# Optimization experiments

Measured on AMD Instinct MI355X. Metric: run time of the kernel, lower is better.

Reference implementation:

```python
import jax, jax.numpy as jnp
import numpy as np

SEQ, BATCH, IN, HID, OUT = 4096, 64, 64, 256, 1


def setup_inputs() -> dict:
    key = jax.random.key(0)
    ks = jax.random.split(key, 7)
    s = 1.0 / np.sqrt(HID)  # torch GRU/Linear init scale
    return {
        "x": jax.random.normal(ks[0], (SEQ, BATCH, IN), dtype=jnp.float32),
        "w_ih": jax.random.uniform(ks[1], (3 * HID, IN), jnp.float32, -s, s),
        "w_hh": jax.random.uniform(ks[2], (3 * HID, HID), jnp.float32, -s, s),
        "b_ih": jax.random.uniform(ks[3], (3 * HID,), jnp.float32, -s, s),
        "b_hh": jax.random.uniform(ks[4], (3 * HID,), jnp.float32, -s, s),
        "fc_w": jax.random.uniform(ks[5], (OUT, HID), jnp.float32, -s, s),
        "fc_b": jax.random.uniform(ks[6], (OUT,), jnp.float32, -s, s),
    }


def _gru(x, w_ih, w_hh, b_ih, b_hh):
    # x: [S, B, I]. Precompute input-side gate projections in one big GEMM.
    xg = jnp.einsum("sbi,gi->sbg", x, w_ih) + b_ih  # [S, B, 3H]
    H = w_hh.shape[1]
    h0 = jnp.zeros((x.shape[1], H), x.dtype)

    def step(h, xt):
        hg = h @ w_hh.T + b_hh  # [B, 3H]
        xr, xz, xn = jnp.split(xt, 3, axis=-1)
        hr, hz, hn = jnp.split(hg, 3, axis=-1)
        r = jax.nn.sigmoid(xr + hr)
        z = jax.nn.sigmoid(xz + hz)
        n = jnp.tanh(xn + r * hn)  # torch GRU: r gates the hidden-side n term
        h_new = (1.0 - z) * n + z * h
        return h_new, h_new

    _, hs = jax.lax.scan(step, h0, xg)  # hs: [S, B, H]
    return hs


def reference(x, w_ih, w_hh, b_ih, b_hh, fc_w, fc_b):
    hs = _gru(x, w_ih, w_hh, b_ih, b_hh)  # [S, B, H]
    out = hs @ fc_w.T + fc_b  # [S, B, OUT]
    # original does .squeeze(0): no-op since S != 1
    return out
```

## Files before the change

### kernel.cpp

```cpp
#include <hip/hip_runtime.h>

#define SEQ  4096
#define NB   64
#define NI   64
#define NH   256

typedef short  bf16x8 __attribute__((ext_vector_type(8)));
typedef short  bf16x4 __attribute__((ext_vector_type(4)));
typedef float  f32x4  __attribute__((ext_vector_type(4)));

__device__ __forceinline__ unsigned short f2bf(float f) {
    union { float f; unsigned u; } v; v.f = f;
    return (unsigned short)((v.u + 0x7fffu + ((v.u >> 16) & 1u)) >> 16);
}
__device__ __forceinline__ float bflo(int p) {
    union { int i; float f; } u; u.i = p << 16; return u.f;
}
__device__ __forceinline__ float bfhi(int p) {
    union { int i; float f; } u; u.i = p & 0xffff0000; return u.f;
}
__device__ __forceinline__ float fast_rcp(float x) { return __builtin_amdgcn_rcpf(x); }
__device__ __forceinline__ float sigm(float x) { return fast_rcp(1.f + __expf(-x)); }
__device__ __forceinline__ float tanh_(float x) {
    x = fminf(15.f, fmaxf(-15.f, x));
    float e = __expf(2.f * x);
    return (e - 1.f) * fast_rcp(e + 1.f);
}
__device__ __forceinline__ f32x4 mfma16(bf16x8 a, bf16x8 b, f32x4 c) {
    return __builtin_amdgcn_mfma_f32_16x16x32_bf16(a, b, c, 0, 0, 0);
}
__device__ __forceinline__ bf16x8 ldfrag(const float* p) {
    float4 a = *(const float4*)p;
    float4 b = *(const float4*)(p + 4);
    bf16x8 r;
    r[0] = (short)f2bf(a.x); r[1] = (short)f2bf(a.y);
    r[2] = (short)f2bf(a.z); r[3] = (short)f2bf(a.w);
    r[4] = (short)f2bf(b.x); r[5] = (short)f2bf(b.y);
    r[6] = (short)f2bf(b.z); r[7] = (short)f2bf(b.w);
    return r;
}

__global__ __launch_bounds__(1024) void xg_pre(
        const float* __restrict__ x, const float* __restrict__ w_ih,
        const float* __restrict__ b_ih, const float* __restrict__ b_hh,
        short* __restrict__ xg, size_t plane, int t0, int ns)
{
    const int tid = threadIdx.x, wv = tid >> 6, lane = tid & 63;
    const int nn = lane & 15, q = lane >> 4;
    const int jb = wv;

    bf16x8 w[3][2];
    float bias[3];
    #pragma unroll
    for (int g = 0; g < 3; ++g) {
        const int row = g * NH + jb * 16 + nn;
        w[g][0] = ldfrag(w_ih + row * NI + q * 8);
        w[g][1] = ldfrag(w_ih + row * NI + 32 + q * 8);
        bias[g] = b_ih[row] + (g < 2 ? b_hh[row] : 0.f);
    }

    const int NT = ns * 4;
    for (int rt = blockIdx.x; rt < NT; rt += gridDim.x) {
        const float* xr = x + ((size_t)t0 * NB + (size_t)rt * 16 + nn) * NI + q * 8;
        bf16x8 a0 = ldfrag(xr);
        bf16x8 a1 = ldfrag(xr + 32);
        #pragma unroll
        for (int g = 0; g < 3; ++g) {
            f32x4 acc = {0.f, 0.f, 0.f, 0.f};
            acc = mfma16(a0, w[g][0], acc);
            acc = mfma16(a1, w[g][1], acc);
            bf16x4 v;
            #pragma unroll
            for (int m = 0; m < 4; ++m) v[m] = (short)f2bf(acc[m] + bias[g]);
            *(bf16x4*)(xg + (size_t)g * plane +
                       (((size_t)rt * 16 + jb) * 64 + lane) * 4) = v;
        }
    }
}

__global__ __launch_bounds__(1024, 4) void gru_rec(
        const short* __restrict__ xg, size_t plane,
        const float* __restrict__ w_hh,
        const float* __restrict__ b_hh,
        const float* __restrict__ fc_w,
        const float* __restrict__ fc_b,
        float* __restrict__ out,
        float* __restrict__ hcar,
        int t0, int ns)
{
    __shared__ short wlds[65536];
    __shared__ short abuf[8192];
    __shared__ short fcwl[4096];
    __shared__ float oring[1024];

    const int tid = threadIdx.x, wv = tid >> 6, lane = tid & 63;
    const int nn = lane & 15, q = lane >> 4;
    const int bc = blockIdx.x, bbase = bc * 16;

    bf16x8 wr[8], wz[8];
    #pragma unroll
    for (int c = 0; c < 8; ++c)
        wr[c] = ldfrag(w_hh + (0 * NH + wv * 16 + nn) * NH + c * 32 + q * 8);
    #pragma unroll
    for (int c = 0; c < 8; ++c)
        wz[c] = ldfrag(w_hh + (1 * NH + wv * 16 + nn) * NH + c * 32 + q * 8);
    #pragma unroll
    for (int c = 0; c < 8; ++c) {
        bf16x8 f = ldfrag(w_hh + (2 * NH + wv * 16 + nn) * NH + c * 32 + q * 8);
        *(bf16x8*)(wlds + (wv * 8 + c) * 512 + lane * 8) = f;
    }
    if (wv < 8) {
        bf16x8 f = 0;
        if (nn == 0) f = ldfrag(fc_w + wv * 32 + q * 8);
        *(bf16x8*)(fcwl + wv * 512 + lane * 8) = f;
    }
    const float bhn = b_hh[2 * NH + wv * 16 + nn];
    const float fcb = fc_b[0];

    f32x4 hp = {0.f, 0.f, 0.f, 0.f};
    if (t0 == 0) {
        ((int4*)abuf)[tid] = make_int4(0, 0, 0, 0);
    } else {
        #pragma unroll
        for (int m = 0; m < 4; ++m)
            hp[m] = hcar[(size_t)(bbase + q * 4 + m) * NH + wv * 16 + nn];
        const int f = tid * 4, b = f >> 8, k0 = f & 255;
        float4 v = *(const float4*)(hcar + (size_t)(bbase + b) * NH + k0);
        bf16x4 s; s[0] = (short)f2bf(v.x); s[1] = (short)f2bf(v.y);
        s[2] = (short)f2bf(v.z); s[3] = (short)f2bf(v.w);
        *(bf16x4*)(abuf + (k0 >> 5) * 512 + (((k0 >> 3) & 3) * 16 + b) * 8 + (k0 & 7)) = s;
    }

    const int j = wv * 16 + nn;
    const int koff = (j >> 5) * 512 + ((j >> 3) & 3) * 128 + (j & 7) + q * 32;
    const short* xgp = xg + ((size_t)(bc * 16 + wv) * 64 + lane) * 4;
    __syncthreads();

    for (int t = 0; t < ns; ++t) {
        const int cur = t & 1, nxt = cur ^ 1;

        int2 gx = *(const int2*)(xgp);
        int2 gz = *(const int2*)(xgp + plane);
        int2 gn = *(const int2*)(xgp + 2 * plane);
        xgp += 16384;

        if ((t & 31) == 1 && t >= 33 && tid < 512) {
            const int s0 = t - 33;
            out[((size_t)(t0 + s0 + (tid >> 4))) * NB + bbase + (tid & 15)] =
                oring[(((s0 >> 5) & 1) << 9) + (tid >> 4) * 16 + (tid & 15)];
        }

        const bool isfc = (t > 0) && (wv == (t & 15));
        f32x4 ar = {0.f,0.f,0.f,0.f}, az = {0.f,0.f,0.f,0.f};
        f32x4 an = {0.f,0.f,0.f,0.f}, afc = {0.f,0.f,0.f,0.f};
        const short* ab = abuf + cur * 4096;
        #pragma unroll
        for (int c = 0; c < 8; ++c) {
            bf16x8 av = *(const bf16x8*)(ab + c * 512 + lane * 8);
            ar = mfma16(av, wr[c], ar);
            az = mfma16(av, wz[c], az);
            bf16x8 wnf = *(const bf16x8*)(wlds + (wv * 8 + c) * 512 + lane * 8);
            an = mfma16(av, wnf, an);
            if (isfc) {
                bf16x8 ff = *(const bf16x8*)(fcwl + c * 512 + lane * 8);
                afc = mfma16(av, ff, afc);
            }
        }
        if (isfc && nn == 0) {
            const int s = t - 1;
            f32x4 v;
            #pragma unroll
            for (int m = 0; m < 4; ++m) v[m] = afc[m] + fcb;
            *(f32x4*)(oring + (((s >> 5) & 1) << 9) + ((s & 31) << 4) + q * 4) = v;
        }

        const float xr4[4] = { bflo(gx.x), bfhi(gx.x), bflo(gx.y), bfhi(gx.y) };
        const float xz4[4] = { bflo(gz.x), bfhi(gz.x), bflo(gz.y), bfhi(gz.y) };
        const float xn4[4] = { bflo(gn.x), bfhi(gn.x), bflo(gn.y), bfhi(gn.y) };

        short* hw = abuf + nxt * 4096 + koff;
        #pragma unroll
        for (int m = 0; m < 4; ++m) {
            float r_ = sigm(ar[m] + xr4[m]);
            float z_ = sigm(az[m] + xz4[m]);
            float n_ = tanh_(fmaf(r_, an[m] + bhn, xn4[m]));
            float h_ = n_ + z_ * (hp[m] - n_);
            hp[m] = h_;
            hw[m * 8] = (short)f2bf(h_);
        }
        __syncthreads();
    }

    if (wv == 0) {
        const short* ab = abuf + (ns & 1) * 4096;
        f32x4 afc = {0.f, 0.f, 0.f, 0.f};
        #pragma unroll
        for (int c = 0; c < 8; ++c)
            afc = mfma16(*(const bf16x8*)(ab + c * 512 + lane * 8),
                         *(const bf16x8*)(fcwl + c * 512 + lane * 8), afc);
        if (nn == 0) {
            const int s = ns - 1;
            f32x4 v;
            #pragma unroll
            for (int m = 0; m < 4; ++m) v[m] = afc[m] + fcb;
            *(f32x4*)(oring + (((s >> 5) & 1) << 9) + ((s & 31) << 4) + q * 4) = v;
        }
    }
    __syncthreads();
    if (tid < 512) {
        const int s0 = ns - 32;
        out[((size_t)(t0 + s0 + (tid >> 4))) * NB + bbase + (tid & 15)] =
            oring[(((s0 >> 5) & 1) << 9) + (tid >> 4) * 16 + (tid & 15)];
    }
    #pragma unroll
    for (int m = 0; m < 4; ++m)
        hcar[(size_t)(bbase + q * 4 + m) * NH + wv * 16 + nn] = hp[m];
}

extern "C" void kernel_launch(void* const* d_in, const int* in_sizes, int n_in,
                              void* d_out, int out_size, void* d_ws, size_t ws_size,
                              hipStream_t stream) {
    (void)in_sizes; (void)n_in; (void)out_size;
    const float* x    = (const float*)d_in[0];
    const float* w_ih = (const float*)d_in[1];
    const float* w_hh = (const float*)d_in[2];
    const float* b_ih = (const float*)d_in[3];
    const float* b_hh = (const float*)d_in[4];
    const float* fc_w = (const float*)d_in[5];
    const float* fc_b = (const float*)d_in[6];
    float* out  = (float*)d_out;
    float* hcar = (float*)d_ws;
    short* xg   = (short*)((char*)d_ws + 65536);

    const size_t per_step = (size_t)NB * 3 * NH * 2;
    long avail = (long)ws_size - 65536;
    int spc = 64;
    if (avail >= (long)per_step * 64) {
        spc = (int)((avail / (long)per_step) / 64) * 64;
        if (spc > SEQ) spc = SEQ;
    }
    for (int t0 = 0; t0 < SEQ; t0 += spc) {
        int ns = (SEQ - t0 < spc) ? (SEQ - t0) : spc;
        size_t plane = (size_t)spc * 16384;
        xg_pre<<<dim3(2048), dim3(1024), 0, stream>>>(x, w_ih, b_ih, b_hh,
                                                      xg, plane, t0, ns);
        gru_rec<<<dim3(4), dim3(1024), 0, stream>>>(xg, plane, w_hh, b_hh,
                                                    fc_w, fc_b, out, hcar,
                                                    t0, ns);
    }
}
```

Before: 6.925 ms.

## Halve recurrent block to 8 waves, two hidden tiles per wave, prefetch xg

The recurrent GRU kernel now runs 512 threads per block instead of 1024. Each wave computes two 16-column hidden tiles, holding r/z weights for both tiles and one n-gate tile in registers, with the other n tile kept in LDS. Fewer waves per block should make the per-step __syncthreads barrier cheaper, and the xg gate inputs for the next step are now prefetched one step ahead so their global-load latency overlaps the MFMA work. The cost is more registers per thread and longer serial per-wave work on each step.

```diff
diff --git a/kernel.cpp b/kernel.cpp
--- a/kernel.cpp
+++ b/kernel.cpp
@@ -78,7 +78,7 @@
     }
 }
 
-__global__ __launch_bounds__(1024, 4) void gru_rec(
+__global__ __launch_bounds__(512, 2) void gru_rec(
         const short* __restrict__ xg, size_t plane,
         const float* __restrict__ w_hh,
         const float* __restrict__ b_hh,
@@ -88,79 +88,110 @@
         float* __restrict__ hcar,
         int t0, int ns)
 {
-    __shared__ short wlds[65536];
-    __shared__ short abuf[8192];
-    __shared__ short fcwl[4096];
-    __shared__ float oring[1024];
+    __shared__ __attribute__((aligned(16))) short wnlds[32768];
+    __shared__ __attribute__((aligned(16))) short abuf[8192];
+    __shared__ __attribute__((aligned(16))) short fcwl[4096];
+    __shared__ __attribute__((aligned(16))) float oring[1024];
 
     const int tid = threadIdx.x, wv = tid >> 6, lane = tid & 63;
     const int nn = lane & 15, q = lane >> 4;
     const int bc = blockIdx.x, bbase = bc * 16;
 
-    bf16x8 wr[8], wz[8];
+    bf16x8 wr[2][8], wz[2][8], wn0[8];
+    #pragma unroll
+    for (int p = 0; p < 2; ++p) {
+        const int row = (wv * 2 + p) * 16 + nn;
+        #pragma unroll
+        for (int c = 0; c < 8; ++c) {
+            wr[p][c] = ldfrag(w_hh + (0 * NH + row) * NH + c * 32 + q * 8);
+            wz[p][c] = ldfrag(w_hh + (1 * NH + row) * NH + c * 32 + q * 8);
+        }
+    }
     #pragma unroll
     for (int c = 0; c < 8; ++c)
-        wr[c] = ldfrag(w_hh + (0 * NH + wv * 16 + nn) * NH + c * 32 + q * 8);
-    #pragma unroll
-    for (int c = 0; c < 8; ++c)
-        wz[c] = ldfrag(w_hh + (1 * NH + wv * 16 + nn) * NH + c * 32 + q * 8);
+        wn0[c] = ldfrag(w_hh + (2 * NH + (wv * 2) * 16 + nn) * NH + c * 32 + q * 8);
     #pragma unroll
     for (int c = 0; c < 8; ++c) {
-        bf16x8 f = ldfrag(w_hh + (2 * NH + wv * 16 + nn) * NH + c * 32 + q * 8);
-        *(bf16x8*)(wlds + (wv * 8 + c) * 512 + lane * 8) = f;
-    }
-    if (wv < 8) {
+        bf16x8 f = ldfrag(w_hh + (2 * NH + (wv * 2 + 1) * 16 + nn) * NH + c * 32 + q * 8);
+        *(bf16x8*)(wnlds + (wv * 8 + c) * 512 + lane * 8) = f;
+    }
+    {
         bf16x8 f = 0;
         if (nn == 0) f = ldfrag(fc_w + wv * 32 + q * 8);
         *(bf16x8*)(fcwl + wv * 512 + lane * 8) = f;
     }
-    const float bhn = b_hh[2 * NH + wv * 16 + nn];
-    const float fcb = fc_b[0];
-
-    f32x4 hp = {0.f, 0.f, 0.f, 0.f};
+    const float bhn0 = b_hh[2 * NH + (wv * 2) * 16 + nn];
+    const float bhn1 = b_hh[2 * NH + (wv * 2 + 1) * 16 + nn];
+    const float fcb  = fc_b[0];
+
+    f32x4 hp0 = {0.f, 0.f, 0.f, 0.f}, hp1 = {0.f, 0.f, 0.f, 0.f};
     if (t0 == 0) {
-        ((int4*)abuf)[tid] = make_int4(0, 0, 0, 0);
+        ((int4*)abuf)[tid]       = make_int4(0, 0, 0, 0);
+        ((int4*)abuf)[tid + 512] = make_int4(0, 0, 0, 0);
     } else {
         #pragma unroll
-        for (int m = 0; m < 4; ++m)
-            hp[m] = hcar[(size_t)(bbase + q * 4 + m) * NH + wv * 16 + nn];
-        const int f = tid * 4, b = f >> 8, k0 = f & 255;
-        float4 v = *(const float4*)(hcar + (size_t)(bbase + b) * NH + k0);
-        bf16x4 s; s[0] = (short)f2bf(v.x); s[1] = (short)f2bf(v.y);
-        s[2] = (short)f2bf(v.z); s[3] = (short)f2bf(v.w);
-        *(bf16x4*)(abuf + (k0 >> 5) * 512 + (((k0 >> 3) & 3) * 16 + b) * 8 + (k0 & 7)) = s;
-    }
-
-    const int j = wv * 16 + nn;
-    const int koff = (j >> 5) * 512 + ((j >> 3) & 3) * 128 + (j & 7) + q * 32;
-    const short* xgp = xg + ((size_t)(bc * 16 + wv) * 64 + lane) * 4;
+        for (int m = 0; m < 4; ++m) {
+            hp0[m] = hcar[(size_t)(bbase + q * 4 + m) * NH + (wv * 2) * 16 + nn];
+            hp1[m] = hcar[(size_t)(bbase + q * 4 + m) * NH + (wv * 2 + 1) * 16 + nn];
+        }
+        #pragma unroll
+        for (int i = 0; i < 2; ++i) {
+            const int f = (tid + i * 512) * 4, b = f >> 8, k0 = f & 255;
+            float4 v = *(const float4*)(hcar + (size_t)(bbase + b) * NH + k0);
+            bf16x4 s; s[0] = (short)f2bf(v.x); s[1] = (short)f2bf(v.y);
+            s[2] = (short)f2bf(v.z); s[3] = (short)f2bf(v.w);
+            *(bf16x4*)(abuf + (k0 >> 5) * 512 + (((k0 >> 3) & 3) * 16 + b) * 8 + (k0 & 7)) = s;
+        }
+    }
+
+    const int j0 = wv * 32 + nn, j1 = j0 + 16;
+    const int koff0 = (j0 >> 5) * 512 + ((j0 >> 3) & 3) * 128 + (j0 & 7) + q * 32;
+    const int koff1 = (j1 >> 5) * 512 + ((j1 >> 3) & 3) * 128 + (j1 & 7) + q * 32;
+    const short* xgp = xg + (((size_t)bc * 16 + wv * 2) * 64 + lane) * 4;
     __syncthreads();
+
+    int2 pr0 = *(const int2*)(xgp);
+    int2 pr1 = *(const int2*)(xgp + 256);
+    int2 pz0 = *(const int2*)(xgp + plane);
+    int2 pz1 = *(const int2*)(xgp + plane + 256);
+    int2 pn0 = *(const int2*)(xgp + 2 * plane);
+    int2 pn1 = *(const int2*)(xgp + 2 * plane + 256);
 
     for (int t = 0; t < ns; ++t) {
         const int cur = t & 1, nxt = cur ^ 1;
 
-        int2 gx = *(const int2*)(xgp);
-        int2 gz = *(const int2*)(xgp + plane);
-        int2 gn = *(const int2*)(xgp + 2 * plane);
-        xgp += 16384;
-
-        if ((t & 31) == 1 && t >= 33 && tid < 512) {
+        const int2 gr0 = pr0, gr1 = pr1, gz0 = pz0, gz1 = pz1;
+        const int2 gn0 = pn0, gn1 = pn1;
+        const short* xq = xgp + ((t + 1 < ns) ? 16384 : 0);
+        pr0 = *(const int2*)(xq);
+        pr1 = *(const int2*)(xq + 256);
+        pz0 = *(const int2*)(xq + plane);
+        pz1 = *(const int2*)(xq + plane + 256);
+        pn0 = *(const int2*)(xq + 2 * plane);
+        pn1 = *(const int2*)(xq + 2 * plane + 256);
+        xgp = xq;
+
+        if ((t & 31) == 1 && t >= 33) {
             const int s0 = t - 33;
             out[((size_t)(t0 + s0 + (tid >> 4))) * NB + bbase + (tid & 15)] =
                 oring[(((s0 >> 5) & 1) << 9) + (tid >> 4) * 16 + (tid & 15)];
         }
 
-        const bool isfc = (t > 0) && (wv == (t & 15));
-        f32x4 ar = {0.f,0.f,0.f,0.f}, az = {0.f,0.f,0.f,0.f};
-        f32x4 an = {0.f,0.f,0.f,0.f}, afc = {0.f,0.f,0.f,0.f};
+        const bool isfc = (t > 0) && (wv == (t & 7));
+        f32x4 ar0 = {0.f,0.f,0.f,0.f}, az0 = {0.f,0.f,0.f,0.f}, an0 = {0.f,0.f,0.f,0.f};
+        f32x4 ar1 = {0.f,0.f,0.f,0.f}, az1 = {0.f,0.f,0.f,0.f}, an1 = {0.f,0.f,0.f,0.f};
+        f32x4 afc = {0.f,0.f,0.f,0.f};
         const short* ab = abuf + cur * 4096;
         #pragma unroll
         for (int c = 0; c < 8; ++c) {
             bf16x8 av = *(const bf16x8*)(ab + c * 512 + lane * 8);
-            ar = mfma16(av, wr[c], ar);
-            az = mfma16(av, wz[c], az);
-            bf16x8 wnf = *(const bf16x8*)(wlds + (wv * 8 + c) * 512 + lane * 8);
-            an = mfma16(av, wnf, an);
+            ar0 = mfma16(av, wr[0][c], ar0);
+            az0 = mfma16(av, wz[0][c], az0);
+            an0 = mfma16(av, wn0[c], an0);
+            ar1 = mfma16(av, wr[1][c], ar1);
+            az1 = mfma16(av, wz[1][c], az1);
+            bf16x8 wnf = *(const bf16x8*)(wnlds + (wv * 8 + c) * 512 + lane * 8);
+            an1 = mfma16(av, wnf, an1);
             if (isfc) {
                 bf16x8 ff = *(const bf16x8*)(fcwl + c * 512 + lane * 8);
                 afc = mfma16(av, ff, afc);
@@ -174,19 +205,35 @@
             *(f32x4*)(oring + (((s >> 5) & 1) << 9) + ((s & 31) << 4) + q * 4) = v;
         }
 
-        const float xr4[4] = { bflo(gx.x), bfhi(gx.x), bflo(gx.y), bfhi(gx.y) };
-        const float xz4[4] = { bflo(gz.x), bfhi(gz.x), bflo(gz.y), bfhi(gz.y) };
-        const float xn4[4] = { bflo(gn.x), bfhi(gn.x), bflo(gn.y), bfhi(gn.y) };
-
-        short* hw = abuf + nxt * 4096 + koff;
-        #pragma unroll
-        for (int m = 0; m < 4; ++m) {
-            float r_ = sigm(ar[m] + xr4[m]);
-            float z_ = sigm(az[m] + xz4[m]);
-            float n_ = tanh_(fmaf(r_, an[m] + bhn, xn4[m]));
-            float h_ = n_ + z_ * (hp[m] - n_);
-            hp[m] = h_;
-            hw[m * 8] = (short)f2bf(h_);
+        {
+            const float xr4[4] = { bflo(gr0.x), bfhi(gr0.x), bflo(gr0.y), bfhi(gr0.y) };
+            const float xz4[4] = { bflo(gz0.x), bfhi(gz0.x), bflo(gz0.y), bfhi(gz0.y) };
+            const float xn4[4] = { bflo(gn0.x), bfhi(gn0.x), bflo(gn0.y), bfhi(gn0.y) };
+            short* hw = abuf + nxt * 4096 + koff0;
+            #pragma unroll
+            for (int m = 0; m < 4; ++m) {
+                float r_ = sigm(ar0[m] + xr4[m]);
+                float z_ = sigm(az0[m] + xz4[m]);
+                float n_ = tanh_(fmaf(r_, an0[m] + bhn0, xn4[m]));
+                float h_ = n_ + z_ * (hp0[m] - n_);
+                hp0[m] = h_;
+                hw[m * 8] = (short)f2bf(h_);
+            }
+        }
+        {
+            const float xr4[4] = { bflo(gr1.x), bfhi(gr1.x), bflo(gr1.y), bfhi(gr1.y) };
+            const float xz4[4] = { bflo(gz1.x), bfhi(gz1.x), bflo(gz1.y), bfhi(gz1.y) };
+            const float xn4[4] = { bflo(gn1.x), bfhi(gn1.x), bflo(gn1.y), bfhi(gn1.y) };
+            short* hw = abuf + nxt * 4096 + koff1;
+            #pragma unroll
+            for (int m = 0; m < 4; ++m) {
+                float r_ = sigm(ar1[m] + xr4[m]);
+                float z_ = sigm(az1[m] + xz4[m]);
+                float n_ = tanh_(fmaf(r_, an1[m] + bhn1, xn4[m]));
+                float h_ = n_ + z_ * (hp1[m] - n_);
+                hp1[m] = h_;
+                hw[m * 8] = (short)f2bf(h_);
+            }
         }
         __syncthreads();
     }
@@ -207,14 +254,16 @@
         }
     }
     __syncthreads();
-    if (tid < 512) {
+    {
         const int s0 = ns - 32;
         out[((size_t)(t0 + s0 + (tid >> 4))) * NB + bbase + (tid & 15)] =
             oring[(((s0 >> 5) & 1) << 9) + (tid >> 4) * 16 + (tid & 15)];
     }
     #pragma unroll
-    for (int m = 0; m < 4; ++m)
-        hcar[(size_t)(bbase + q * 4 + m) * NH + wv * 16 + nn] = hp[m];
+    for (int m = 0; m < 4; ++m) {
+        hcar[(size_t)(bbase + q * 4 + m) * NH + wv * 32 + nn]      = hp0[m];
+        hcar[(size_t)(bbase + q * 4 + m) * NH + wv * 32 + 16 + nn] = hp1[m];
+    }
 }
 
 extern "C" void kernel_launch(void* const* d_in, const int* in_sizes, int n_in,
@@ -244,8 +293,8 @@
         size_t plane = (size_t)spc * 16384;
         xg_pre<<<dim3(2048), dim3(1024), 0, stream>>>(x, w_ih, b_ih, b_hh,
                                                       xg, plane, t0, ns);
-        gru_rec<<<dim3(4), dim3(1024), 0, stream>>>(xg, plane, w_hh, b_hh,
-                                                    fc_w, fc_b, out, hcar,
-                                                    t0, ns);
-    }
-}
+        gru_rec<<<dim3(4), dim3(512), 0, stream>>>(xg, plane, w_hh, b_hh,
+                                                   fc_w, fc_b, out, hcar,
+                                                   t0, ns);
+    }
+}
```

New measurement: 9.960 ms. 1.44x slower.
